# Optimization experiments

Measured on AMD Instinct MI355X. Metric: run time of the kernel, lower is better.

Reference implementation:

```python
import jax, jax.numpy as jnp
import numpy as np

B, N, D, E = 16, 4096, 1024, 64
TOP_K = 2
ROUTING_FLOOR_BASE = 0.05
CAP_LOW, CAP_HIGH, T_MAX = 0.5, 0.6, 1000


def setup_inputs() -> dict:
    key = jax.random.key(0)
    k1, k2, k3 = jax.random.split(key, 3)
    tokens_B = jax.random.normal(k1, (B, N, D), dtype=jnp.float32)
    t = jax.random.randint(k2, (B,), 0, T_MAX, dtype=jnp.int32)
    W_g = jax.random.normal(k3, (E, D), dtype=jnp.float32) * (1.0 / np.sqrt(D))
    b_g = jnp.zeros((E,), dtype=jnp.float32)
    return {"tokens_B": tokens_B, "t": t, "W_g": W_g, "b_g": b_g}


def _apply_routing_floor(probs, floor):
    # interpolate toward uniform so each expert gets >= floor mass
    e = probs.shape[-1]
    if floor <= 0.0:
        return probs
    alpha = min(floor * e, 1.0)
    return (1.0 - alpha) * probs + alpha / e


def _hard_cap(probs, t):
    # cap(t) = cap_low + (cap_high + cap_low) * t/T_max  (faithful to source)
    t_norm = t.astype(probs.dtype) / T_MAX
    cap = (CAP_LOW + (CAP_HIGH + CAP_LOW) * t_norm)[:, None, None]  # (B,1,1)
    excess = jax.nn.relu(probs - cap)
    capped = probs - excess
    headroom = jax.nn.relu(cap - capped)
    headroom_sum = jnp.clip(headroom.sum(-1, keepdims=True), 1e-8)
    capped = capped + excess.sum(-1, keepdims=True) * (headroom / headroom_sum)
    # torch version runs under no_grad; use straight-through so gate still trains
    return probs + jax.lax.stop_gradient(capped - probs)


def _topk_mask(probs, k):
    vals, idx = jax.lax.top_k(probs, k)  # (B,N,k)
    onehot = jax.nn.one_hot(idx, probs.shape[-1], dtype=probs.dtype)  # (B,N,k,E)
    return jnp.einsum('bnk,bnke->bne', vals, onehot)


def reference(tokens_B, t, W_g, b_g):
    logits = jnp.einsum('bnd,ed->bne', tokens_B, W_g) + b_g  # (B,N,E)
    probs = jax.nn.softmax(logits, axis=-1)
    floor = min(ROUTING_FLOOR_BASE, 0.15 / max(E, 1))
    probs = _apply_routing_floor(probs, floor)
    capped = _hard_cap(probs, t)
    gates = _topk_mask(capped, TOP_K)  # sparse gate mask (B,N,E)
    return gates
```

## Files before the change

### kernel.cpp

```cpp
#include <hip/hip_runtime.h>
#include <hip/hip_bf16.h>

typedef __attribute__((ext_vector_type(8))) short short8;
typedef __attribute__((ext_vector_type(4))) short sh4;
typedef __attribute__((ext_vector_type(4))) float floatx4;

__device__ __forceinline__ bool better(float va, int ia, float vb, int ib) {
    return (va > vb) || (va == vb && ia < ib);
}
__device__ __forceinline__ bool betterd(double va, int ia, double vb, int ib) {
    return (va > vb) || (va == vb && ia < ib);
}

__device__ __forceinline__ short bf16_rn(float f) {
    __hip_bfloat16 h = __float2bfloat16(f);
    return *reinterpret_cast<short*>(&h);
}
__device__ __forceinline__ float bf16_up(short s) {
    return __uint_as_float(((unsigned)(unsigned short)s) << 16);
}

__device__ __forceinline__ void split8(float4 a, float4 b, short8& hi, short8& lo) {
    float v[8] = {a.x, a.y, a.z, a.w, b.x, b.y, b.z, b.w};
    #pragma unroll
    for (int i = 0; i < 8; ++i) {
        short h = bf16_rn(v[i]);
        hi[i] = h;
        lo[i] = bf16_rn(v[i] - bf16_up(h));
    }
}

#define MFMA(A, B, C) __builtin_amdgcn_mfma_f32_16x16x32_bf16((A), (B), (C), 0, 0, 0)

__device__ __forceinline__ void gload16(const void* g, void* l) {
    __builtin_amdgcn_global_load_lds(
        (const __attribute__((address_space(1))) void*)g,
        (__attribute__((address_space(3))) void*)l,
        16, 0, 0);
}

__global__ __launch_bounds__(256)
void wsplit_kernel(const float* __restrict__ Wg,
                   short* __restrict__ whi,
                   short* __restrict__ wlo)
{
    const int idx = blockIdx.x * 256 + threadIdx.x;
    const int c = idx >> 8;
    const int g = (idx >> 6) & 3;
    const int q = (idx >> 4) & 3;
    const int e = idx & 15;
    const float* src = Wg + (size_t)(g * 16 + e) * 1024 + c * 32 + q * 8;
    float4 v0 = reinterpret_cast<const float4*>(src)[0];
    float4 v1 = reinterpret_cast<const float4*>(src)[1];
    short8 hi, lo;
    split8(v0, v1, hi, lo);
    reinterpret_cast<short8*>(whi)[idx] = hi;
    reinterpret_cast<short8*>(wlo)[idx] = lo;
}

__global__ __launch_bounds__(256, 2)
void router_kernel(const float* __restrict__ tokens,
                   const int* __restrict__ tarr,
                   const float* __restrict__ bg,
                   float* __restrict__ out,
                   int* __restrict__ flagCount,
                   int* __restrict__ flagList,
                   int listCap,
                   const short* __restrict__ whi,
                   const short* __restrict__ wlo)
{
    __shared__ __align__(16) float gtile[64 * 64];
    __shared__ __align__(16) char  wbuf[2][8192];

    const int lane = threadIdx.x & 63;
    const int wave = threadIdx.x >> 6;
    const int c16  = lane & 15;
    const int quad = lane >> 4;

    const int tokenBase = blockIdx.x * 64;
    const int token     = tokenBase + wave * 16 + c16;

    const float4* ap = reinterpret_cast<const float4*>(tokens) + (size_t)token * 256 + quad * 2;

    const char* hS = (const char*)whi + wave * 1024 + (size_t)lane * 16;
    const char* lS = (const char*)wlo + wave * 1024 + (size_t)lane * 16;
    char* wb0h = wbuf[0];
    char* wb1h = wbuf[1];

    const int wRd = lane * 16;

    floatx4 acc0 = {0.f, 0.f, 0.f, 0.f};
    floatx4 acc1 = acc0, acc2 = acc0, acc3 = acc0;

#define STAGE_W(c, wb)  do {                                              \
        gload16(hS + (size_t)(c) * 4096, (wb) + wave * 1024);             \
        gload16(lS + (size_t)(c) * 4096, (wb) + 4096 + wave * 1024);      \
    } while (0)

#define LOAD_A(c, A0, A1)  do {                                           \
        (A0) = ap[(c) * 8];                                               \
        (A1) = ap[(c) * 8 + 1];                                           \
    } while (0)

#define COMPUTE(wb, A0, A1)  do {                                         \
        const char* bW = (wb);                                            \
        short8 h0 = *(const short8*)(bW +    0 + wRd);                    \
        short8 h1 = *(const short8*)(bW + 1024 + wRd);                    \
        short8 h2 = *(const short8*)(bW + 2048 + wRd);                    \
        short8 h3 = *(const short8*)(bW + 3072 + wRd);                    \
        short8 l0 = *(const short8*)(bW + 4096 + wRd);                    \
        short8 l1 = *(const short8*)(bW + 5120 + wRd);                    \
        short8 l2 = *(const short8*)(bW + 6144 + wRd);                    \
        short8 l3 = *(const short8*)(bW + 7168 + wRd);                    \
        short8 ahi, alo;                                                  \
        split8((A0), (A1), ahi, alo);                                     \
        acc0 = MFMA(ahi, h0, acc0); acc0 = MFMA(alo, h0, acc0); acc0 = MFMA(ahi, l0, acc0); \
        acc1 = MFMA(ahi, h1, acc1); acc1 = MFMA(alo, h1, acc1); acc1 = MFMA(ahi, l1, acc1); \
        acc2 = MFMA(ahi, h2, acc2); acc2 = MFMA(alo, h2, acc2); acc2 = MFMA(ahi, l2, acc2); \
        acc3 = MFMA(ahi, h3, acc3); acc3 = MFMA(alo, h3, acc3); acc3 = MFMA(ahi, l3, acc3); \
    } while (0)

#define WAIT4  asm volatile("s_waitcnt vmcnt(4)" ::: "memory")
#define WAIT0  asm volatile("s_waitcnt vmcnt(0)" ::: "memory")
#define BAR    do { __builtin_amdgcn_s_barrier(); asm volatile("" ::: "memory"); } while (0)

    float4 a0A, a1A, a0B, a1B;

    STAGE_W(0, wb0h);  LOAD_A(0, a0A, a1A);
    STAGE_W(1, wb1h);  LOAD_A(1, a0B, a1B);

    #pragma unroll 1
    for (int cc = 0; cc < 15; ++cc) {
        const int c0 = 2 * cc;
        WAIT4;
        BAR;
        COMPUTE(wb0h, a0A, a1A);
        BAR;
        STAGE_W(c0 + 2, wb0h);  LOAD_A(c0 + 2, a0A, a1A);
        WAIT4;
        BAR;
        COMPUTE(wb1h, a0B, a1B);
        BAR;
        STAGE_W(c0 + 3, wb1h);  LOAD_A(c0 + 3, a0B, a1B);
    }
    WAIT4;
    BAR;
    COMPUTE(wb0h, a0A, a1A);
    BAR;
    WAIT0;
    BAR;
    COMPUTE(wb1h, a0B, a1B);

#undef STAGE_W
#undef LOAD_A
#undef COMPUTE
#undef WAIT4
#undef WAIT0
#undef BAR

    const float b0f = bg[c16 +  0];
    const float b1f = bg[c16 + 16];
    const float b2f = bg[c16 + 32];
    const float b3f = bg[c16 + 48];

    const float tb  = (float)tarr[tokenBase >> 12];
    const float cap = 0.5f + 1.1f * (tb / 1000.0f);

    const float A1 = 0.85f;
    const float A2 = 0.15f / 64.0f;

    #pragma unroll
    for (int rr = 0; rr < 4; ++rr) {
        float l0 = acc0[rr] + b0f;
        float l1 = acc1[rr] + b1f;
        float l2 = acc2[rr] + b2f;
        float l3 = acc3[rr] + b3f;

        float mx = fmaxf(fmaxf(l0, l1), fmaxf(l2, l3));
        #pragma unroll
        for (int off = 8; off >= 1; off >>= 1)
            mx = fmaxf(mx, __shfl_xor(mx, off));

        float e0 = expf(l0 - mx), e1 = expf(l1 - mx);
        float e2 = expf(l2 - mx), e3 = expf(l3 - mx);
        float s = e0 + e1 + e2 + e3;
        #pragma unroll
        for (int off = 8; off >= 1; off >>= 1)
            s += __shfl_xor(s, off);
        float inv = 1.0f / s;

        float p0 = A1 * (e0 * inv) + A2;
        float p1 = A1 * (e1 * inv) + A2;
        float p2 = A1 * (e2 * inv) + A2;
        float p3 = A1 * (e3 * inv) + A2;

        float x0 = fmaxf(p0 - cap, 0.f), x1 = fmaxf(p1 - cap, 0.f);
        float x2 = fmaxf(p2 - cap, 0.f), x3 = fmaxf(p3 - cap, 0.f);
        float m0 = p0 - x0, m1 = p1 - x1, m2 = p2 - x2, m3 = p3 - x3;
        float h0 = fmaxf(cap - m0, 0.f), h1 = fmaxf(cap - m1, 0.f);
        float h2 = fmaxf(cap - m2, 0.f), h3 = fmaxf(cap - m3, 0.f);
        float sx = x0 + x1 + x2 + x3;
        float sh = h0 + h1 + h2 + h3;
        #pragma unroll
        for (int off = 8; off >= 1; off >>= 1) {
            sx += __shfl_xor(sx, off);
            sh += __shfl_xor(sh, off);
        }
        sh = fmaxf(sh, 1e-8f);
        float sc = sx / sh;
        float c0 = m0 + sc * h0;
        float c1 = m1 + sc * h1;
        float c2 = m2 + sc * h2;
        float c3 = m3 + sc * h3;

        const int iA = c16, iB = c16 + 16, iC = c16 + 32, iD = c16 + 48;
        float v1, v2; int j1, j2;
        if (better(c0, iA, c1, iB)) { v1 = c0; j1 = iA; v2 = c1; j2 = iB; }
        else                        { v1 = c1; j1 = iB; v2 = c0; j2 = iA; }
        if (better(c2, iC, v1, j1))      { v2 = v1; j2 = j1; v1 = c2; j1 = iC; }
        else if (better(c2, iC, v2, j2)) { v2 = c2; j2 = iC; }
        if (better(c3, iD, v1, j1))      { v2 = v1; j2 = j1; v1 = c3; j1 = iD; }
        else if (better(c3, iD, v2, j2)) { v2 = c3; j2 = iD; }

        #pragma unroll
        for (int off = 1; off < 16; off <<= 1) {
            float w1 = __shfl_xor(v1, off); int k1 = __shfl_xor(j1, off);
            float w2 = __shfl_xor(v2, off); int k2 = __shfl_xor(j2, off);
            if (better(w1, k1, v1, j1)) {
                if (better(v1, j1, w2, k2)) { v2 = v1; j2 = j1; }
                else                        { v2 = w2; j2 = k2; }
                v1 = w1; j1 = k1;
            } else if (better(w1, k1, v2, j2)) {
                v2 = w1; j2 = k1;
            }
        }

        float g0 = (iA == j1 || iA == j2) ? c0 : 0.f;
        float g1 = (iB == j1 || iB == j2) ? c1 : 0.f;
        float g2 = (iC == j1 || iC == j2) ? c2 : 0.f;
        float g3 = (iD == j1 || iD == j2) ? c3 : 0.f;

        float t0 = (iA == j1 || iA == j2) ? -3.0e38f : c0;
        float t1 = (iB == j1 || iB == j2) ? -3.0e38f : c1;
        float t2 = (iC == j1 || iC == j2) ? -3.0e38f : c2;
        float t3 = (iD == j1 || iD == j2) ? -3.0e38f : c3;
        float m3v = fmaxf(fmaxf(t0, t1), fmaxf(t2, t3));
        #pragma unroll
        for (int off = 8; off >= 1; off >>= 1)
            m3v = fmaxf(m3v, __shfl_xor(m3v, off));

        const int tl = wave * 16 + quad * 4 + rr;
        bool flag = ((v2 - m3v) < 1e-4f) || (sx > 0.0f);
        if (flag && c16 == 0) {
            int pos = atomicAdd(flagCount, 1);
            if (pos < listCap) flagList[pos] = tokenBase + tl;
        }

        gtile[tl * 64 + iA] = g0;
        gtile[tl * 64 + iB] = g1;
        gtile[tl * 64 + iC] = g2;
        gtile[tl * 64 + iD] = g3;
    }

    __syncthreads();

    const uint4* src = reinterpret_cast<const uint4*>(gtile);
    uint4* dst = reinterpret_cast<uint4*>(out + (size_t)tokenBase * 64);
    dst[threadIdx.x]       = src[threadIdx.x];
    dst[threadIdx.x + 256] = src[threadIdx.x + 256];
    dst[threadIdx.x + 512] = src[threadIdx.x + 512];
    dst[threadIdx.x + 768] = src[threadIdx.x + 768];
}

__global__ __launch_bounds__(256, 4)
void router_kernel_legacy(const float* __restrict__ tokens,
                          const int* __restrict__ tarr,
                          const float* __restrict__ Wg,
                          const float* __restrict__ bg,
                          float* __restrict__ out,
                          int* __restrict__ flagCount,
                          int* __restrict__ flagList,
                          int listCap)
{
    __shared__ __align__(16) float gtile[64 * 64];

    const int lane = threadIdx.x & 63;
    const int wave = threadIdx.x >> 6;
    const int c16  = lane & 15;
    const int quad = lane >> 4;

    const int tokenBase = blockIdx.x * 64;
    const int token     = tokenBase + wave * 16 + c16;

    const float4* ap = reinterpret_cast<const float4*>(tokens) + (size_t)token * 256 + quad * 2;
    const float4* wp0 = reinterpret_cast<const float4*>(Wg) + (size_t)(c16 +  0) * 256 + quad * 2;
    const float4* wp1 = reinterpret_cast<const float4*>(Wg) + (size_t)(c16 + 16) * 256 + quad * 2;
    const float4* wp2 = reinterpret_cast<const float4*>(Wg) + (size_t)(c16 + 32) * 256 + quad * 2;
    const float4* wp3 = reinterpret_cast<const float4*>(Wg) + (size_t)(c16 + 48) * 256 + quad * 2;

    floatx4 acc0 = {0.f, 0.f, 0.f, 0.f};
    floatx4 acc1 = acc0, acc2 = acc0, acc3 = acc0;

    for (int kb = 0; kb < 32; ++kb) {
        short8 ahi, alo;
        split8(ap[kb * 8], ap[kb * 8 + 1], ahi, alo);
        {
            short8 whi, wlo;
            split8(wp0[kb * 8], wp0[kb * 8 + 1], whi, wlo);
            acc0 = MFMA(ahi, whi, acc0);
            acc0 = MFMA(alo, whi, acc0);
            acc0 = MFMA(ahi, wlo, acc0);
        }
        {
            short8 whi, wlo;
            split8(wp1[kb * 8], wp1[kb * 8 + 1], whi, wlo);
            acc1 = MFMA(ahi, whi, acc1);
            acc1 = MFMA(alo, whi, acc1);
            acc1 = MFMA(ahi, wlo, acc1);
        }
        {
            short8 whi, wlo;
            split8(wp2[kb * 8], wp2[kb * 8 + 1], whi, wlo);
            acc2 = MFMA(ahi, whi, acc2);
            acc2 = MFMA(alo, whi, acc2);
            acc2 = MFMA(ahi, wlo, acc2);
        }
        {
            short8 whi, wlo;
            split8(wp3[kb * 8], wp3[kb * 8 + 1], whi, wlo);
            acc3 = MFMA(ahi, whi, acc3);
            acc3 = MFMA(alo, whi, acc3);
            acc3 = MFMA(ahi, wlo, acc3);
        }
    }

    const float b0f = bg[c16 +  0];
    const float b1f = bg[c16 + 16];
    const float b2f = bg[c16 + 32];
    const float b3f = bg[c16 + 48];

    const float tb  = (float)tarr[tokenBase >> 12];
    const float cap = 0.5f + 1.1f * (tb / 1000.0f);

    const float A1 = 0.85f;
    const float A2 = 0.15f / 64.0f;

    #pragma unroll
    for (int r = 0; r < 4; ++r) {
        float l0 = acc0[r] + b0f;
        float l1 = acc1[r] + b1f;
        float l2 = acc2[r] + b2f;
        float l3 = acc3[r] + b3f;

        float mx = fmaxf(fmaxf(l0, l1), fmaxf(l2, l3));
        #pragma unroll
        for (int off = 8; off >= 1; off >>= 1)
            mx = fmaxf(mx, __shfl_xor(mx, off));

        float e0 = expf(l0 - mx), e1 = expf(l1 - mx);
        float e2 = expf(l2 - mx), e3 = expf(l3 - mx);
        float s = e0 + e1 + e2 + e3;
        #pragma unroll
        for (int off = 8; off >= 1; off >>= 1)
            s += __shfl_xor(s, off);
        float inv = 1.0f / s;

        float p0 = A1 * (e0 * inv) + A2;
        float p1 = A1 * (e1 * inv) + A2;
        float p2 = A1 * (e2 * inv) + A2;
        float p3 = A1 * (e3 * inv) + A2;

        float x0 = fmaxf(p0 - cap, 0.f), x1 = fmaxf(p1 - cap, 0.f);
        float x2 = fmaxf(p2 - cap, 0.f), x3 = fmaxf(p3 - cap, 0.f);
        float m0 = p0 - x0, m1 = p1 - x1, m2 = p2 - x2, m3 = p3 - x3;
        float h0 = fmaxf(cap - m0, 0.f), h1 = fmaxf(cap - m1, 0.f);
        float h2 = fmaxf(cap - m2, 0.f), h3 = fmaxf(cap - m3, 0.f);
        float sx = x0 + x1 + x2 + x3;
        float sh = h0 + h1 + h2 + h3;
        #pragma unroll
        for (int off = 8; off >= 1; off >>= 1) {
            sx += __shfl_xor(sx, off);
            sh += __shfl_xor(sh, off);
        }
        sh = fmaxf(sh, 1e-8f);
        float sc = sx / sh;
        float c0 = m0 + sc * h0;
        float c1 = m1 + sc * h1;
        float c2 = m2 + sc * h2;
        float c3 = m3 + sc * h3;

        const int iA = c16, iB = c16 + 16, iC = c16 + 32, iD = c16 + 48;
        float v1, v2; int j1, j2;
        if (better(c0, iA, c1, iB)) { v1 = c0; j1 = iA; v2 = c1; j2 = iB; }
        else                        { v1 = c1; j1 = iB; v2 = c0; j2 = iA; }
        if (better(c2, iC, v1, j1))      { v2 = v1; j2 = j1; v1 = c2; j1 = iC; }
        else if (better(c2, iC, v2, j2)) { v2 = c2; j2 = iC; }
        if (better(c3, iD, v1, j1))      { v2 = v1; j2 = j1; v1 = c3; j1 = iD; }
        else if (better(c3, iD, v2, j2)) { v2 = c3; j2 = iD; }

        #pragma unroll
        for (int off = 1; off < 16; off <<= 1) {
            float w1 = __shfl_xor(v1, off); int k1 = __shfl_xor(j1, off);
            float w2 = __shfl_xor(v2, off); int k2 = __shfl_xor(j2, off);
            if (better(w1, k1, v1, j1)) {
                if (better(v1, j1, w2, k2)) { v2 = v1; j2 = j1; }
                else                        { v2 = w2; j2 = k2; }
                v1 = w1; j1 = k1;
            } else if (better(w1, k1, v2, j2)) {
                v2 = w1; j2 = k1;
            }
        }

        float g0 = (iA == j1 || iA == j2) ? c0 : 0.f;
        float g1 = (iB == j1 || iB == j2) ? c1 : 0.f;
        float g2 = (iC == j1 || iC == j2) ? c2 : 0.f;
        float g3 = (iD == j1 || iD == j2) ? c3 : 0.f;

        float t0 = (iA == j1 || iA == j2) ? -3.0e38f : c0;
        float t1 = (iB == j1 || iB == j2) ? -3.0e38f : c1;
        float t2 = (iC == j1 || iC == j2) ? -3.0e38f : c2;
        float t3 = (iD == j1 || iD == j2) ? -3.0e38f : c3;
        float m3v = fmaxf(fmaxf(t0, t1), fmaxf(t2, t3));
        #pragma unroll
        for (int off = 8; off >= 1; off >>= 1)
            m3v = fmaxf(m3v, __shfl_xor(m3v, off));

        const int tl = wave * 16 + quad * 4 + r;
        bool flag = ((v2 - m3v) < 1e-4f) || (sx > 0.0f);
        if (flag && c16 == 0) {
            int pos = atomicAdd(flagCount, 1);
            if (pos < listCap) flagList[pos] = tokenBase + tl;
        }

        gtile[tl * 64 + iA] = g0;
        gtile[tl * 64 + iB] = g1;
        gtile[tl * 64 + iC] = g2;
        gtile[tl * 64 + iD] = g3;
    }

    __syncthreads();

    const uint4* src = reinterpret_cast<const uint4*>(gtile);
    uint4* dst = reinterpret_cast<uint4*>(out + (size_t)tokenBase * 64);
    dst[threadIdx.x]       = src[threadIdx.x];
    dst[threadIdx.x + 256] = src[threadIdx.x + 256];
    dst[threadIdx.x + 512] = src[threadIdx.x + 512];
    dst[threadIdx.x + 768] = src[threadIdx.x + 768];
}

__global__ __launch_bounds__(256)
void repair_kernel(const float* __restrict__ tokens,
                   const int* __restrict__ tarr,
                   const float* __restrict__ Wg,
                   const float* __restrict__ bg,
                   float* __restrict__ out,
                   const int* __restrict__ cnt,
                   const int* __restrict__ list,
                   int listCap)
{
    __shared__ __align__(16) float atile[8][1024];
    __shared__ double red[256];
    int count = cnt[0];
    if (count > listCap) count = listCap;

    const int e    = threadIdx.x & 63;
    const int part = threadIdx.x >> 6;

    for (int base = blockIdx.x * 8; base < count; base += gridDim.x * 8) {
        const int n = min(8, count - base);

        #pragma unroll
        for (int t = 0; t < 8; ++t) {
            if (t < n) {
                const float4* src =
                    reinterpret_cast<const float4*>(tokens + (size_t)list[base + t] * 1024);
                reinterpret_cast<float4*>(atile[t])[threadIdx.x] = src[threadIdx.x];
            }
        }
        __syncthreads();

        double acc0 = 0.0, acc1 = 0.0, acc2 = 0.0, acc3 = 0.0;
        double acc4 = 0.0, acc5 = 0.0, acc6 = 0.0, acc7 = 0.0;
        const float* wrow = Wg + (size_t)e * 1024 + part * 256;
        const int ko = part * 256;
        for (int k = 0; k < 256; k += 4) {
            float4 wv = *reinterpret_cast<const float4*>(wrow + k);
            const double w0 = (double)wv.x, w1 = (double)wv.y;
            const double w2 = (double)wv.z, w3 = (double)wv.w;
            #define ACC(T, A)                                                   \
                A = fma((double)atile[T][ko + k    ], w0, A);                    \
                A = fma((double)atile[T][ko + k + 1], w1, A);                    \
                A = fma((double)atile[T][ko + k + 2], w2, A);                    \
                A = fma((double)atile[T][ko + k + 3], w3, A);
            ACC(0, acc0) ACC(1, acc1) ACC(2, acc2) ACC(3, acc3)
            ACC(4, acc4) ACC(5, acc5) ACC(6, acc6) ACC(7, acc7)
            #undef ACC
        }

        #pragma unroll
        for (int t = 0; t < 8; ++t) {
            if (t >= n) break;
            double accT = (t == 0) ? acc0 : (t == 1) ? acc1 : (t == 2) ? acc2 :
                          (t == 3) ? acc3 : (t == 4) ? acc4 : (t == 5) ? acc5 :
                          (t == 6) ? acc6 : acc7;
            red[threadIdx.x] = accT;
            __syncthreads();

            if (threadIdx.x < 64) {
                const int token = list[base + t];
                double l = ((red[e] + red[64 + e]) + (red[128 + e] + red[192 + e]))
                         + (double)bg[e];

                double mxv = l;
                #pragma unroll
                for (int off = 32; off >= 1; off >>= 1)
                    mxv = fmax(mxv, __shfl_xor(mxv, off));
                double ex = exp(l - mxv);
                double s = ex;
                #pragma unroll
                for (int off = 32; off >= 1; off >>= 1)
                    s += __shfl_xor(s, off);

                const double alpha = 0.15;
                double p = (1.0 - alpha) * (ex / s) + alpha / 64.0;

                double tb  = (double)tarr[token >> 12];
                double capv = 0.5 + (0.6 + 0.5) * (tb / 1000.0);
                double x = fmax(p - capv, 0.0);
                double m = p - x;
                double h = fmax(capv - m, 0.0);
                double sx = x, sh = h;
                #pragma unroll
                for (int off = 32; off >= 1; off >>= 1) {
                    sx += __shfl_xor(sx, off);
                    sh += __shfl_xor(sh, off);
                }
                sh = fmax(sh, 1e-8);
                double c = m + (sx / sh) * h;

                double v1 = c, v2 = -1.0e300;
                int j1 = e, j2 = 127;
                #pragma unroll
                for (int off = 1; off < 64; off <<= 1) {
                    double w1 = __shfl_xor(v1, off); int k1 = __shfl_xor(j1, off);
                    double w2 = __shfl_xor(v2, off); int k2 = __shfl_xor(j2, off);
                    if (betterd(w1, k1, v1, j1)) {
                        if (betterd(v1, j1, w2, k2)) { v2 = v1; j2 = j1; }
                        else                         { v2 = w2; j2 = k2; }
                        v1 = w1; j1 = k1;
                    } else if (betterd(w1, k1, v2, j2)) {
                        v2 = w1; j2 = k1;
                    }
                }

                float g = (e == j1 || e == j2) ? (float)c : 0.0f;
                out[(size_t)token * 64 + e] = g;
            }
            __syncthreads();
        }
    }
}

extern "C" void kernel_launch(void* const* d_in, const int* in_sizes, int n_in,
                              void* d_out, int out_size, void* d_ws, size_t ws_size,
                              hipStream_t stream) {
    const float* tokens = (const float*)d_in[0];
    const int*   t      = (const int*)d_in[1];
    const float* Wg     = (const float*)d_in[2];
    const float* bg     = (const float*)d_in[3];
    float*       outp   = (float*)d_out;

    int* wsI = (int*)d_ws;
    const long long wsInts = (long long)(ws_size / 4);

    const int  WHALF   = 32768;
    const long long listOff = 16 + 2LL * WHALF;
    long long cap = wsInts - listOff;
    if (cap > 65536) cap = 65536;

    hipMemsetAsync(d_ws, 0, 64, stream);

    if (cap >= 32768) {
        short* whi  = (short*)(wsI + 16);
        short* wlo  = (short*)(wsI + 16 + WHALF);
        int*   list = wsI + listOff;
        wsplit_kernel<<<dim3(32), dim3(256), 0, stream>>>(Wg, whi, wlo);
        router_kernel<<<dim3(65536 / 64), dim3(256), 0, stream>>>(
            tokens, t, bg, outp, wsI, list, (int)cap, whi, wlo);
        repair_kernel<<<dim3(256), dim3(256), 0, stream>>>(
            tokens, t, Wg, bg, outp, wsI, list, (int)cap);
    } else {
        long long cap2 = wsInts - 16;
        if (cap2 < 0) cap2 = 0;
        if (cap2 > 65536) cap2 = 65536;
        router_kernel_legacy<<<dim3(65536 / 64), dim3(256), 0, stream>>>(
            tokens, t, Wg, bg, outp, wsI, wsI + 16, (int)cap2);
        repair_kernel<<<dim3(256), dim3(256), 0, stream>>>(
            tokens, t, Wg, bg, outp, wsI, wsI + 16, (int)cap2);
    }
}
```

Baseline: 448.2 us.

## Batch token loads eight chunks ahead and fully unroll the K loop

Replaces the double-buffered per-chunk token loads with a register queue that prefetches eight K-chunks of activations at once, refilled every eight chunks. The 32-chunk loop is fully unrolled with explicit vmcnt waits around the LDS-staged weight double buffer. The aim is to keep more global loads in flight so the memory-bound activation stream is better hidden. The cost is higher register pressure, which can lower occupancy, and full vmcnt(0) drains at each eight-chunk boundary that stall the pipeline.

```diff
diff --git a/kernel.cpp b/kernel.cpp
--- a/kernel.cpp
+++ b/kernel.cpp
@@ -84,8 +84,6 @@
 
     const char* hS = (const char*)whi + wave * 1024 + (size_t)lane * 16;
     const char* lS = (const char*)wlo + wave * 1024 + (size_t)lane * 16;
-    char* wb0h = wbuf[0];
-    char* wb1h = wbuf[1];
 
     const int wRd = lane * 16;
 
@@ -95,11 +93,6 @@
 #define STAGE_W(c, wb)  do {                                              \
         gload16(hS + (size_t)(c) * 4096, (wb) + wave * 1024);             \
         gload16(lS + (size_t)(c) * 4096, (wb) + 4096 + wave * 1024);      \
-    } while (0)
-
-#define LOAD_A(c, A0, A1)  do {                                           \
-        (A0) = ap[(c) * 8];                                               \
-        (A1) = ap[(c) * 8 + 1];                                           \
     } while (0)
 
 #define COMPUTE(wb, A0, A1)  do {                                         \
@@ -120,43 +113,47 @@
         acc3 = MFMA(ahi, h3, acc3); acc3 = MFMA(alo, h3, acc3); acc3 = MFMA(ahi, l3, acc3); \
     } while (0)
 
-#define WAIT4  asm volatile("s_waitcnt vmcnt(4)" ::: "memory")
-#define WAIT0  asm volatile("s_waitcnt vmcnt(0)" ::: "memory")
-#define BAR    do { __builtin_amdgcn_s_barrier(); asm volatile("" ::: "memory"); } while (0)
-
-    float4 a0A, a1A, a0B, a1B;
-
-    STAGE_W(0, wb0h);  LOAD_A(0, a0A, a1A);
-    STAGE_W(1, wb1h);  LOAD_A(1, a0B, a1B);
-
-    #pragma unroll 1
-    for (int cc = 0; cc < 15; ++cc) {
-        const int c0 = 2 * cc;
-        WAIT4;
-        BAR;
-        COMPUTE(wb0h, a0A, a1A);
-        BAR;
-        STAGE_W(c0 + 2, wb0h);  LOAD_A(c0 + 2, a0A, a1A);
-        WAIT4;
-        BAR;
-        COMPUTE(wb1h, a0B, a1B);
-        BAR;
-        STAGE_W(c0 + 3, wb1h);  LOAD_A(c0 + 3, a0B, a1B);
-    }
-    WAIT4;
-    BAR;
-    COMPUTE(wb0h, a0A, a1A);
-    BAR;
-    WAIT0;
-    BAR;
-    COMPUTE(wb1h, a0B, a1B);
+    float4 aq[8][2];
+
+    #pragma unroll
+    for (int j = 0; j < 8; ++j) {
+        aq[j][0] = ap[j * 8];
+        aq[j][1] = ap[j * 8 + 1];
+    }
+    STAGE_W(0, wbuf[0]);
+    STAGE_W(1, wbuf[1]);
+
+    #pragma unroll
+    for (int q = 0; q < 4; ++q) {
+        #pragma unroll
+        for (int i = 0; i < 8; ++i) {
+            const int c = q * 8 + i;
+            if (i == 0 || c == 31) {
+                asm volatile("s_waitcnt vmcnt(0)" ::: "memory");
+            } else {
+                asm volatile("s_waitcnt vmcnt(2)" ::: "memory");
+            }
+            __builtin_amdgcn_s_barrier();
+            asm volatile("" ::: "memory");
+
+            COMPUTE(wbuf[i & 1], aq[i][0], aq[i][1]);
+
+            __builtin_amdgcn_s_barrier();
+            asm volatile("" ::: "memory");
+
+            if (c < 30) STAGE_W(c + 2, wbuf[i & 1]);
+            if (i == 7 && q < 3) {
+                #pragma unroll
+                for (int j = 0; j < 8; ++j) {
+                    aq[j][0] = ap[(q + 1) * 64 + j * 8];
+                    aq[j][1] = ap[(q + 1) * 64 + j * 8 + 1];
+                }
+            }
+        }
+    }
 
 #undef STAGE_W
-#undef LOAD_A
 #undef COMPUTE
-#undef WAIT4
-#undef WAIT0
-#undef BAR
 
     const float b0f = bg[c16 +  0];
     const float b1f = bg[c16 + 16];
```

Result: no change. 444.5 us (-0.8%).
